# Optimization experiments

Hardware: AMD Instinct MI355X
Metric: run time of the kernel (lower is better)

## Reference

```python
import jax, jax.numpy as jnp
import numpy as np
import math

EMB = 768
B, S = 8, 2048

def setup_inputs() -> dict:
    key = jax.random.key(0)
    ks = jax.random.split(key, 6)
    q = jax.random.normal(ks[0], (B, S, EMB), dtype=jnp.float32)
    k = jax.random.normal(ks[1], (B, S, EMB), dtype=jnp.float32)
    v = jax.random.normal(ks[2], (B, S, EMB), dtype=jnp.float32)
    mask = jax.random.randint(ks[3], (B, S, S), 0, 2, dtype=jnp.int32)
    # nn.Linear(emb, emb): weight [out, in], bias [out]
    bound = 1.0 / math.sqrt(EMB)
    W = jax.random.uniform(ks[4], (EMB, EMB), minval=-bound, maxval=bound, dtype=jnp.float32)
    b = jax.random.uniform(ks[5], (EMB,), minval=-bound, maxval=bound, dtype=jnp.float32)
    return {"q": q, "k": k, "v": v, "mask": mask, "W": W, "b": b}

def reference(q, k, v, mask, W, b):
    # shared linear projection (torch Linear: x @ W^T + b)
    qp = jnp.einsum('bse,oe->bso', q, W) + b
    kp = jnp.einsum('bse,oe->bso', k, W) + b
    vp = jnp.einsum('bse,oe->bso', v, W) + b
    scores = jnp.einsum('bqe,bke->bqk', qp, kp) / math.sqrt(EMB)  # [B,S,S]
    scores = jnp.where(mask == 1, -jnp.inf, scores)
    attn = jax.nn.softmax(scores, axis=-1)
    return jnp.einsum('bqk,bke->bqe', attn, vp)
```

## Files before the change

### kernel.cpp

```cpp
#include <hip/hip_runtime.h>
#include <hip/hip_bf16.h>
#include <stdint.h>

#define B_ 8
#define S_ 2048
#define E_ 768

typedef __attribute__((ext_vector_type(4))) float f32x4;
typedef __attribute__((ext_vector_type(8))) short bf16x8;

#define TILE_USH (256 * 32)

__device__ __forceinline__ unsigned pk2bf(float x, float y) {
  unsigned r;
  asm("v_cvt_pk_bf16_f32 %0, %1, %2" : "=v"(r) : "v"(x), "v"(y));
  return r;
}

__device__ __forceinline__ void gll16(const void* g, void* l) {
  __builtin_amdgcn_global_load_lds((const __attribute__((address_space(1))) void*)g,
                                   (__attribute__((address_space(3))) void*)l, 16, 0, 0);
}

__device__ __forceinline__ void stage_op(const char* Gb, int ld, int kt,
                                         unsigned short* Ls, int tid) {
#pragma unroll
  for (int i = 0; i < 2; ++i) {
    const unsigned lin = (unsigned)i * 8192u + (unsigned)tid * 16u;
    const unsigned row = lin >> 6;
    const unsigned chunk = (lin >> 4) & 3u;
    const unsigned sw = (chunk ^ ((row >> 1) & 3u)) << 4;
    gll16(Gb + (size_t)row * ld + (size_t)kt * 64 + sw, (char*)Ls + lin);
  }
}

__device__ __forceinline__ void ldsA8(const unsigned short* As, int wm, int lane,
                                      bf16x8 (&af)[8]) {
  const unsigned ksw = (unsigned)(lane >> 4);
#pragma unroll
  for (int m = 0; m < 8; ++m) {
    const unsigned row = (unsigned)(wm * 128 + m * 16 + (lane & 15));
    const unsigned off = row * 64 + ((ksw ^ ((row >> 1) & 3u)) << 4);
    af[m] = *reinterpret_cast<const bf16x8*>((const char*)As + off);
  }
}

__device__ __forceinline__ void ldsB2(const unsigned short* Bs, int wn, int n0, int lane,
                                      bf16x8 (&bf)[2]) {
  const unsigned ksw = (unsigned)(lane >> 4);
#pragma unroll
  for (int j = 0; j < 2; ++j) {
    const unsigned row = (unsigned)(wn * 64 + (n0 + j) * 16 + (lane & 15));
    const unsigned off = row * 64 + ((ksw ^ ((row >> 1) & 3u)) << 4);
    bf[j] = *reinterpret_cast<const bf16x8*>((const char*)Bs + off);
  }
}

__device__ __forceinline__ void gemm_pipe32(const char* Ab, const char* Bb, int ldA, int ldB,
                                            int NT, unsigned short* AsAll, unsigned short* BsAll,
                                            int tid, int wm, int wn, int lane,
                                            f32x4 (&acc)[8][4]) {
#pragma unroll
  for (int t = 0; t < 3; ++t) {
    stage_op(Ab, ldA, t, AsAll + t * TILE_USH, tid);
    stage_op(Bb, ldB, t, BsAll + t * TILE_USH, tid);
  }
  asm volatile("s_waitcnt vmcnt(8)" ::: "memory");
  __builtin_amdgcn_s_barrier();
  __builtin_amdgcn_sched_barrier(0);
  for (int kt = 0; kt < NT; ++kt) {
    const int bk = kt & 3;
    const unsigned short* As = AsAll + bk * TILE_USH;
    const unsigned short* Bs = BsAll + bk * TILE_USH;
    const int bs = (kt + 3) & 3;
    bf16x8 af[8], b01[2], b23[2];
    ldsA8(As, wm, lane, af);
    ldsB2(Bs, wn, 0, lane, b01);
    if (kt + 3 < NT) stage_op(Ab, ldA, kt + 3, AsAll + bs * TILE_USH, tid);
    __builtin_amdgcn_s_barrier();
    asm volatile("s_waitcnt lgkmcnt(0)" ::: "memory");
    __builtin_amdgcn_sched_barrier(0);
    __builtin_amdgcn_s_setprio(1);
#pragma unroll
    for (int m = 0; m < 8; ++m) {
      acc[m][0] = __builtin_amdgcn_mfma_f32_16x16x32_bf16(af[m], b01[0], acc[m][0], 0, 0, 0);
      acc[m][1] = __builtin_amdgcn_mfma_f32_16x16x32_bf16(af[m], b01[1], acc[m][1], 0, 0, 0);
    }
    __builtin_amdgcn_s_setprio(0);
    __builtin_amdgcn_s_barrier();
    ldsB2(Bs, wn, 2, lane, b23);
    if (kt + 3 < NT) stage_op(Bb, ldB, kt + 3, BsAll + bs * TILE_USH, tid);
    __builtin_amdgcn_s_barrier();
    asm volatile("s_waitcnt lgkmcnt(0)" ::: "memory");
    __builtin_amdgcn_sched_barrier(0);
    __builtin_amdgcn_s_setprio(1);
#pragma unroll
    for (int m = 0; m < 8; ++m) {
      acc[m][2] = __builtin_amdgcn_mfma_f32_16x16x32_bf16(af[m], b23[0], acc[m][2], 0, 0, 0);
      acc[m][3] = __builtin_amdgcn_mfma_f32_16x16x32_bf16(af[m], b23[1], acc[m][3], 0, 0, 0);
    }
    __builtin_amdgcn_s_setprio(0);
    if (kt + 1 < NT) {
      if (kt + 3 < NT)       asm volatile("s_waitcnt vmcnt(8)" ::: "memory");
      else if (kt + 3 == NT) asm volatile("s_waitcnt vmcnt(4)" ::: "memory");
      else                   asm volatile("s_waitcnt vmcnt(0)" ::: "memory");
      __builtin_amdgcn_s_barrier();
      __builtin_amdgcn_sched_barrier(0);
    }
  }
}

__global__ __launch_bounds__(256) void k_cvt(const float* __restrict__ q,
                                             const float* __restrict__ k,
                                             const float* __restrict__ v,
                                             const float* __restrict__ W,
                                             const int* __restrict__ mask,
                                             unsigned short* __restrict__ qb,
                                             unsigned short* __restrict__ kb,
                                             unsigned short* __restrict__ vb,
                                             unsigned short* __restrict__ Wb,
                                             unsigned long long* __restrict__ mwords) {
  const int y = blockIdx.y;
  if (y == 4) {
    const int nchunks = B_ * S_ * (S_ / 256);
    const int lane = threadIdx.x & 63;
    const int wave = (blockIdx.x * 256 + threadIdx.x) >> 6;
    const int nw = gridDim.x * 4;
    int c = wave;
    for (; c + 3 * nw < nchunks; c += 4 * nw) {
      int4 v0 = *reinterpret_cast<const int4*>(&mask[(size_t)c * 256 + lane * 4]);
      int4 v1 = *reinterpret_cast<const int4*>(&mask[(size_t)(c + nw) * 256 + lane * 4]);
      int4 v2 = *reinterpret_cast<const int4*>(&mask[(size_t)(c + 2 * nw) * 256 + lane * 4]);
      int4 v3 = *reinterpret_cast<const int4*>(&mask[(size_t)(c + 3 * nw) * 256 + lane * 4]);
      unsigned long long a0 = __ballot(v0.x == 1), a1 = __ballot(v0.y == 1);
      unsigned long long a2 = __ballot(v0.z == 1), a3 = __ballot(v0.w == 1);
      unsigned long long b0 = __ballot(v1.x == 1), b1 = __ballot(v1.y == 1);
      unsigned long long b2 = __ballot(v1.z == 1), b3 = __ballot(v1.w == 1);
      unsigned long long c0 = __ballot(v2.x == 1), c1 = __ballot(v2.y == 1);
      unsigned long long c2 = __ballot(v2.z == 1), c3 = __ballot(v2.w == 1);
      unsigned long long d0 = __ballot(v3.x == 1), d1 = __ballot(v3.y == 1);
      unsigned long long d2 = __ballot(v3.z == 1), d3 = __ballot(v3.w == 1);
      if (lane == 0) {
        *reinterpret_cast<ulonglong2*>(&mwords[(size_t)c * 4]) = make_ulonglong2(a0, a1);
        *reinterpret_cast<ulonglong2*>(&mwords[(size_t)c * 4 + 2]) = make_ulonglong2(a2, a3);
        *reinterpret_cast<ulonglong2*>(&mwords[(size_t)(c + nw) * 4]) = make_ulonglong2(b0, b1);
        *reinterpret_cast<ulonglong2*>(&mwords[(size_t)(c + nw) * 4 + 2]) = make_ulonglong2(b2, b3);
        *reinterpret_cast<ulonglong2*>(&mwords[(size_t)(c + 2 * nw) * 4]) = make_ulonglong2(c0, c1);
        *reinterpret_cast<ulonglong2*>(&mwords[(size_t)(c + 2 * nw) * 4 + 2]) = make_ulonglong2(c2, c3);
        *reinterpret_cast<ulonglong2*>(&mwords[(size_t)(c + 3 * nw) * 4]) = make_ulonglong2(d0, d1);
        *reinterpret_cast<ulonglong2*>(&mwords[(size_t)(c + 3 * nw) * 4 + 2]) = make_ulonglong2(d2, d3);
      }
    }
    for (; c < nchunks; c += nw) {
      int4 v0 = *reinterpret_cast<const int4*>(&mask[(size_t)c * 256 + lane * 4]);
      unsigned long long a0 = __ballot(v0.x == 1), a1 = __ballot(v0.y == 1);
      unsigned long long a2 = __ballot(v0.z == 1), a3 = __ballot(v0.w == 1);
      if (lane == 0) {
        *reinterpret_cast<ulonglong2*>(&mwords[(size_t)c * 4]) = make_ulonglong2(a0, a1);
        *reinterpret_cast<ulonglong2*>(&mwords[(size_t)c * 4 + 2]) = make_ulonglong2(a2, a3);
      }
    }
    return;
  }
  const float* src = (y == 0) ? q : (y == 1) ? k : (y == 2) ? v : W;
  unsigned short* dst = (y == 0) ? qb : (y == 1) ? kb : (y == 2) ? vb : Wb;
  const int n4 = (y < 3) ? (B_ * S_ * E_ / 4) : (E_ * E_ / 4);
  const int stride = gridDim.x * 256;
  const float4* s4 = reinterpret_cast<const float4*>(src);
  uint2* d2 = reinterpret_cast<uint2*>(dst);
  int i = blockIdx.x * 256 + threadIdx.x;
  for (; i + 3 * stride < n4; i += 4 * stride) {
    float4 f0 = s4[i];
    float4 f1 = s4[i + stride];
    float4 f2 = s4[i + 2 * stride];
    float4 f3 = s4[i + 3 * stride];
    d2[i]              = make_uint2(pk2bf(f0.x, f0.y), pk2bf(f0.z, f0.w));
    d2[i + stride]     = make_uint2(pk2bf(f1.x, f1.y), pk2bf(f1.z, f1.w));
    d2[i + 2 * stride] = make_uint2(pk2bf(f2.x, f2.y), pk2bf(f2.z, f2.w));
    d2[i + 3 * stride] = make_uint2(pk2bf(f3.x, f3.y), pk2bf(f3.z, f3.w));
  }
  for (; i < n4; i += stride) {
    float4 f0 = s4[i];
    d2[i] = make_uint2(pk2bf(f0.x, f0.y), pk2bf(f0.z, f0.w));
  }
}

__global__ __launch_bounds__(512, 1) void k_projb(const unsigned short* __restrict__ Xb,
                                                  const unsigned short* __restrict__ Wb,
                                                  const float* __restrict__ bias,
                                                  unsigned short* __restrict__ qp,
                                                  unsigned short* __restrict__ kp,
                                                  unsigned short* __restrict__ vp) {
  __shared__ __attribute__((aligned(16))) unsigned short AsAll[4 * TILE_USH];
  __shared__ __attribute__((aligned(16))) unsigned short BsAll[4 * TILE_USH];
  const int tid = threadIdx.x, lane = tid & 63, wid = tid >> 6;
  const int wm = wid >> 2, wn = wid & 3;
  const int c0 = blockIdx.x * 256, r0 = blockIdx.y * 256, z = blockIdx.z;
  const unsigned short* X = Xb + (size_t)z * (B_ * S_ * E_);
  unsigned short* O = (z == 0) ? qp : ((z == 1) ? kp : vp);

  const char* Ab = (const char*)(X + (size_t)r0 * E_);
  const char* Bb = (const char*)(Wb + (size_t)c0 * E_);
  f32x4 acc[8][4] = {};
  gemm_pipe32(Ab, Bb, E_ * 2, E_ * 2, E_ / 32, AsAll, BsAll, tid, wm, wn, lane, acc);

  float bcol[4];
#pragma unroll
  for (int n = 0; n < 4; ++n) bcol[n] = bias[c0 + wn * 64 + n * 16 + (lane & 15)];
#pragma unroll
  for (int m = 0; m < 8; ++m)
#pragma unroll
    for (int r = 0; r < 4; ++r) {
      const int row = r0 + wm * 128 + m * 16 + (lane >> 4) * 4 + r;
#pragma unroll
      for (int n = 0; n < 4; ++n) {
        const int col = c0 + wn * 64 + n * 16 + (lane & 15);
        O[(size_t)row * E_ + col] = (unsigned short)pk2bf(acc[m][n][r] + bcol[n], 0.f);
      }
    }
}

__global__ __launch_bounds__(256) void k_vtrans(const unsigned short* __restrict__ vp,
                                                unsigned short* __restrict__ vpT) {
  __shared__ __attribute__((aligned(16))) unsigned short t[64][72];
  const int tid = threadIdx.x;
  const int st = blockIdx.x;
  const int ot = blockIdx.y;
  const int b = blockIdx.z;
#pragma unroll
  for (int i = 0; i < 2; ++i) {
    int f = i * 256 + tid;
    int s = f >> 3, c8 = f & 7;
    uint4 vv = *reinterpret_cast<const uint4*>(
        &vp[((size_t)b * S_ + st * 64 + s) * E_ + ot * 64 + c8 * 8]);
    *reinterpret_cast<uint4*>(&t[s][c8 * 8]) = vv;
  }
  __syncthreads();
  const int o = tid >> 2;
  const int sb = (tid & 3) * 16;
  unsigned p[8];
#pragma unroll
  for (int j = 0; j < 8; ++j)
    p[j] = (unsigned)t[sb + 2 * j][o] | ((unsigned)t[sb + 2 * j + 1][o] << 16);
  uint4 w0 = make_uint4(p[0], p[1], p[2], p[3]);
  uint4 w1 = make_uint4(p[4], p[5], p[6], p[7]);
  size_t ob = ((size_t)b * E_ + ot * 64 + o) * S_ + st * 64 + sb;
  *reinterpret_cast<uint4*>(&vpT[ob]) = w0;
  *reinterpret_cast<uint4*>(&vpT[ob + 8]) = w1;
}

__global__ __launch_bounds__(512, 1) void k_scores(const unsigned short* __restrict__ qp,
                                                   const unsigned short* __restrict__ kp,
                                                   const unsigned long long* __restrict__ mwords,
                                                   unsigned short* __restrict__ P,
                                                   float* __restrict__ rowsum) {
  __shared__ __attribute__((aligned(16))) unsigned short AsAll[4 * TILE_USH];
  __shared__ __attribute__((aligned(16))) unsigned short BsAll[4 * TILE_USH];
  __shared__ float rlds[256][4];
  const int tid = threadIdx.x, lane = tid & 63, wid = tid >> 6;
  const int wm = wid >> 2, wn = wid & 3;
  const int yt = blockIdx.x, qt = blockIdx.y, b = blockIdx.z;
  const char* Ab = (const char*)(qp + ((size_t)b * S_ + qt * 256) * E_);
  const char* Bb = (const char*)(kp + ((size_t)b * S_ + yt * 256) * E_);
  f32x4 acc[8][4] = {};
  gemm_pipe32(Ab, Bb, E_ * 2, E_ * 2, E_ / 32, AsAll, BsAll, tid, wm, wn, lane, acc);

  const float SC = (float)(1.4426950408889634 / 27.712812921102035);
#pragma unroll
  for (int m = 0; m < 8; ++m)
#pragma unroll
    for (int r = 0; r < 4; ++r) {
      const int rloc = wm * 128 + m * 16 + (lane >> 4) * 4 + r;
      const int grow = qt * 256 + rloc;
      const size_t rowoff = ((size_t)b * S_ + grow) * S_;
      const unsigned long long mw =
          mwords[(((size_t)b * S_ + grow) * 8 + yt) * 4 + (lane & 3)];
      const int shb = wn * 16 + ((lane & 15) >> 2);
      const int cbase = yt * 256 + wn * 64 + (lane & 15);
      float radd = 0.f;
#pragma unroll
      for (int n = 0; n < 4; ++n) {
        float pv = ((mw >> (shb + n * 4)) & 1ull)
                       ? 0.f
                       : __builtin_amdgcn_exp2f(acc[m][n][r] * SC);
        radd += pv;
        P[rowoff + cbase + n * 16] = (unsigned short)pk2bf(pv, 0.f);
      }
      float vsum = radd;
      vsum += __shfl_xor(vsum, 1);
      vsum += __shfl_xor(vsum, 2);
      vsum += __shfl_xor(vsum, 4);
      vsum += __shfl_xor(vsum, 8);
      if ((lane & 15) == 0) rlds[rloc][wn] = vsum;
    }
  __syncthreads();
  if (tid < 256) {
    rowsum[(size_t)yt * (B_ * S_) + (size_t)b * S_ + qt * 256 + tid] =
        (rlds[tid][0] + rlds[tid][1]) + (rlds[tid][2] + rlds[tid][3]);
  }
}

__global__ __launch_bounds__(256) void k_invrs(const float* __restrict__ rowsum,
                                               float* __restrict__ inv_rs) {
  int i = blockIdx.x * 256 + threadIdx.x;
  float t = 0.f;
#pragma unroll
  for (int g = 0; g < 8; ++g) t += rowsum[(size_t)g * (B_ * S_) + i];
  inv_rs[i] = 1.0f / t;
}

__global__ __launch_bounds__(512, 1) void k_pv(const unsigned short* __restrict__ P,
                                               const unsigned short* __restrict__ vpT,
                                               const float* __restrict__ inv_rs,
                                               float* __restrict__ out) {
  __shared__ __attribute__((aligned(16))) unsigned short AsAll[4 * TILE_USH];
  __shared__ __attribute__((aligned(16))) unsigned short BsAll[4 * TILE_USH];
  const int tid = threadIdx.x, lane = tid & 63, wid = tid >> 6;
  const int wm = wid >> 2, wn = wid & 3;
  const int yt = blockIdx.x, mt = blockIdx.y, b = blockIdx.z;
  const char* Ab = (const char*)(P + ((size_t)b * S_ + mt * 256) * S_);
  const char* Bb = (const char*)(vpT + ((size_t)b * E_ + yt * 256) * S_);
  f32x4 acc[8][4] = {};
  gemm_pipe32(Ab, Bb, S_ * 2, S_ * 2, S_ / 32, AsAll, BsAll, tid, wm, wn, lane, acc);

#pragma unroll
  for (int m = 0; m < 8; ++m)
#pragma unroll
    for (int r = 0; r < 4; ++r) {
      const int grow = mt * 256 + wm * 128 + m * 16 + (lane >> 4) * 4 + r;
      const float inv = inv_rs[b * S_ + grow];
#pragma unroll
      for (int n = 0; n < 4; ++n) {
        const int col = yt * 256 + wn * 64 + n * 16 + (lane & 15);
        out[((size_t)b * S_ + grow) * E_ + col] = acc[m][n][r] * inv;
      }
    }
}

extern "C" void kernel_launch(void* const* d_in, const int* in_sizes, int n_in,
                              void* d_out, int out_size, void* d_ws, size_t ws_size,
                              hipStream_t stream) {
  const float* q = (const float*)d_in[0];
  const float* k = (const float*)d_in[1];
  const float* v = (const float*)d_in[2];
  const int* mask = (const int*)d_in[3];
  const float* W = (const float*)d_in[4];
  const float* bias = (const float*)d_in[5];
  float* out = (float*)d_out;
  char* ws = (char*)d_ws;

  unsigned short* qb = (unsigned short*)(ws + 0);
  unsigned short* kb = (unsigned short*)(ws + 25165824);
  unsigned short* vb = (unsigned short*)(ws + 50331648);
  unsigned short* Wb = (unsigned short*)(ws + 75497472);
  unsigned short* qp = (unsigned short*)(ws + 76677120);
  unsigned short* kp = (unsigned short*)(ws + 101842944);
  unsigned short* vpT = (unsigned short*)(ws + 127008768);
  unsigned short* P = (unsigned short*)(ws + 0);
  float* rowsum = (float*)(ws + 75497472);
  float* inv_rs = (float*)(ws + 76546048);
  unsigned short* vp_tmp = (unsigned short*)d_out;
  unsigned long long* mwords =
      (unsigned long long*)((char*)d_out + 25165824);
  (void)in_sizes; (void)n_in; (void)out_size; (void)ws_size;

  dim3 blk(256, 1, 1);
  dim3 blk2(512, 1, 1);
  k_cvt<<<dim3(512, 5, 1), blk, 0, stream>>>(q, k, v, W, mask, qb, kb, vb, Wb, mwords);
  k_projb<<<dim3(3, 64, 3), blk2, 0, stream>>>(qb, Wb, bias, qp, kp, vp_tmp);
  k_vtrans<<<dim3(32, 12, 8), blk, 0, stream>>>(vp_tmp, vpT);
  k_scores<<<dim3(8, 8, 8), blk2, 0, stream>>>(qp, kp, mwords, P, rowsum);
  k_invrs<<<dim3(64, 1, 1), blk, 0, stream>>>(rowsum, inv_rs);
  k_pv<<<dim3(3, 8, 8), blk2, 0, stream>>>(P, vpT, inv_rs, out);
}
```

Before: 327.0 us.

## Switch GEMMs to 128x128 tiles with double buffering and 3 blocks per CU

Replaces the 256x256-tile, 512-thread, 4-stage GEMM pipeline with a 128x128 tile, 256-thread, 2-stage double-buffered loop used by the projection, scores and PV kernels. Grids grow fourfold and launch bounds allow 3 blocks per CU, aiming for more occupancy and better wave balance across CUs. Mask word indexing and the rowsum partial count (8 to 16) are adjusted to the new tile width. The trade is lower arithmetic intensity per tile, more global/L2 traffic, and a shallower prefetch that fully drains vmcnt each iteration.

```diff
diff --git a/kernel.cpp b/kernel.cpp
--- a/kernel.cpp
+++ b/kernel.cpp
@@ -9,7 +9,6 @@
 typedef __attribute__((ext_vector_type(4))) float f32x4;
 typedef __attribute__((ext_vector_type(8))) short bf16x8;
 
-#define TILE_USH (256 * 32)
 
 __device__ __forceinline__ unsigned pk2bf(float x, float y) {
   unsigned r;
@@ -22,88 +21,67 @@
                                    (__attribute__((address_space(3))) void*)l, 16, 0, 0);
 }
 
-__device__ __forceinline__ void stage_op(const char* Gb, int ld, int kt,
-                                         unsigned short* Ls, int tid) {
+__device__ __forceinline__ void gemm128(const char* __restrict__ Ab,
+                                        const char* __restrict__ Bb,
+                                        int ldA, int ldB, int NT,
+                                        unsigned short* As, unsigned short* Bs,
+                                        int tid, int wm, int wn, int lane,
+                                        f32x4 (&acc)[4][4]) {
+  unsigned sA[2], sB[2], lin2[2];
 #pragma unroll
   for (int i = 0; i < 2; ++i) {
-    const unsigned lin = (unsigned)i * 8192u + (unsigned)tid * 16u;
-    const unsigned row = lin >> 6;
-    const unsigned chunk = (lin >> 4) & 3u;
-    const unsigned sw = (chunk ^ ((row >> 1) & 3u)) << 4;
-    gll16(Gb + (size_t)row * ld + (size_t)kt * 64 + sw, (char*)Ls + lin);
-  }
-}
-
-__device__ __forceinline__ void ldsA8(const unsigned short* As, int wm, int lane,
-                                      bf16x8 (&af)[8]) {
-  const unsigned ksw = (unsigned)(lane >> 4);
-#pragma unroll
-  for (int m = 0; m < 8; ++m) {
-    const unsigned row = (unsigned)(wm * 128 + m * 16 + (lane & 15));
-    const unsigned off = row * 64 + ((ksw ^ ((row >> 1) & 3u)) << 4);
-    af[m] = *reinterpret_cast<const bf16x8*>((const char*)As + off);
-  }
-}
-
-__device__ __forceinline__ void ldsB2(const unsigned short* Bs, int wn, int n0, int lane,
-                                      bf16x8 (&bf)[2]) {
-  const unsigned ksw = (unsigned)(lane >> 4);
-#pragma unroll
-  for (int j = 0; j < 2; ++j) {
-    const unsigned row = (unsigned)(wn * 64 + (n0 + j) * 16 + (lane & 15));
-    const unsigned off = row * 64 + ((ksw ^ ((row >> 1) & 3u)) << 4);
-    bf[j] = *reinterpret_cast<const bf16x8*>((const char*)Bs + off);
-  }
-}
-
-__device__ __forceinline__ void gemm_pipe32(const char* Ab, const char* Bb, int ldA, int ldB,
-                                            int NT, unsigned short* AsAll, unsigned short* BsAll,
-                                            int tid, int wm, int wn, int lane,
-                                            f32x4 (&acc)[8][4]) {
-#pragma unroll
-  for (int t = 0; t < 3; ++t) {
-    stage_op(Ab, ldA, t, AsAll + t * TILE_USH, tid);
-    stage_op(Bb, ldB, t, BsAll + t * TILE_USH, tid);
-  }
-  asm volatile("s_waitcnt vmcnt(8)" ::: "memory");
+    const unsigned lin = (unsigned)i * 4096u + (unsigned)tid * 16u;
+    const unsigned row = lin >> 6, ch = (lin >> 4) & 3u;
+    const unsigned sw = (ch ^ ((row >> 1) & 3u)) << 4;
+    sA[i] = row * (unsigned)ldA + sw;
+    sB[i] = row * (unsigned)ldB + sw;
+    lin2[i] = lin;
+  }
+  unsigned aoff[4], boff[4];
+#pragma unroll
+  for (int m = 0; m < 4; ++m) {
+    unsigned row = (unsigned)(wm * 64 + m * 16 + (lane & 15));
+    aoff[m] = row * 64 + ((((unsigned)lane >> 4) ^ ((row >> 1) & 3u)) << 4);
+    row = (unsigned)(wn * 64 + m * 16 + (lane & 15));
+    boff[m] = row * 64 + ((((unsigned)lane >> 4) ^ ((row >> 1) & 3u)) << 4);
+  }
+#pragma unroll
+  for (int i = 0; i < 2; ++i) {
+    gll16(Ab + sA[i], (char*)As + lin2[i]);
+    gll16(Bb + sB[i], (char*)Bs + lin2[i]);
+  }
+  asm volatile("s_waitcnt vmcnt(0)" ::: "memory");
   __builtin_amdgcn_s_barrier();
   __builtin_amdgcn_sched_barrier(0);
   for (int kt = 0; kt < NT; ++kt) {
-    const int bk = kt & 3;
-    const unsigned short* As = AsAll + bk * TILE_USH;
-    const unsigned short* Bs = BsAll + bk * TILE_USH;
-    const int bs = (kt + 3) & 3;
-    bf16x8 af[8], b01[2], b23[2];
-    ldsA8(As, wm, lane, af);
-    ldsB2(Bs, wn, 0, lane, b01);
-    if (kt + 3 < NT) stage_op(Ab, ldA, kt + 3, AsAll + bs * TILE_USH, tid);
-    __builtin_amdgcn_s_barrier();
+    const char* Ac = (const char*)As + (kt & 1) * 8192;
+    const char* Bc = (const char*)Bs + (kt & 1) * 8192;
+    char* An = (char*)As + ((kt + 1) & 1) * 8192;
+    char* Bn = (char*)Bs + ((kt + 1) & 1) * 8192;
+    if (kt + 1 < NT) {
+      const size_t ko = (size_t)(kt + 1) * 64;
+#pragma unroll
+      for (int i = 0; i < 2; ++i) {
+        gll16(Ab + sA[i] + ko, An + lin2[i]);
+        gll16(Bb + sB[i] + ko, Bn + lin2[i]);
+      }
+    }
+    bf16x8 af[4], bf[4];
+#pragma unroll
+    for (int m = 0; m < 4; ++m) af[m] = *reinterpret_cast<const bf16x8*>(Ac + aoff[m]);
+#pragma unroll
+    for (int n = 0; n < 4; ++n) bf[n] = *reinterpret_cast<const bf16x8*>(Bc + boff[n]);
     asm volatile("s_waitcnt lgkmcnt(0)" ::: "memory");
     __builtin_amdgcn_sched_barrier(0);
     __builtin_amdgcn_s_setprio(1);
 #pragma unroll
-    for (int m = 0; m < 8; ++m) {
-      acc[m][0] = __builtin_amdgcn_mfma_f32_16x16x32_bf16(af[m], b01[0], acc[m][0], 0, 0, 0);
-      acc[m][1] = __builtin_amdgcn_mfma_f32_16x16x32_bf16(af[m], b01[1], acc[m][1], 0, 0, 0);
-    }
-    __builtin_amdgcn_s_setprio(0);
-    __builtin_amdgcn_s_barrier();
-    ldsB2(Bs, wn, 2, lane, b23);
-    if (kt + 3 < NT) stage_op(Bb, ldB, kt + 3, BsAll + bs * TILE_USH, tid);
-    __builtin_amdgcn_s_barrier();
-    asm volatile("s_waitcnt lgkmcnt(0)" ::: "memory");
-    __builtin_amdgcn_sched_barrier(0);
-    __builtin_amdgcn_s_setprio(1);
-#pragma unroll
-    for (int m = 0; m < 8; ++m) {
-      acc[m][2] = __builtin_amdgcn_mfma_f32_16x16x32_bf16(af[m], b23[0], acc[m][2], 0, 0, 0);
-      acc[m][3] = __builtin_amdgcn_mfma_f32_16x16x32_bf16(af[m], b23[1], acc[m][3], 0, 0, 0);
-    }
+    for (int m = 0; m < 4; ++m)
+#pragma unroll
+      for (int n = 0; n < 4; ++n)
+        acc[m][n] = __builtin_amdgcn_mfma_f32_16x16x32_bf16(af[m], bf[n], acc[m][n], 0, 0, 0);
     __builtin_amdgcn_s_setprio(0);
     if (kt + 1 < NT) {
-      if (kt + 3 < NT)       asm volatile("s_waitcnt vmcnt(8)" ::: "memory");
-      else if (kt + 3 == NT) asm volatile("s_waitcnt vmcnt(4)" ::: "memory");
-      else                   asm volatile("s_waitcnt vmcnt(0)" ::: "memory");
+      asm volatile("s_waitcnt vmcnt(0)" ::: "memory");
       __builtin_amdgcn_s_barrier();
       __builtin_amdgcn_sched_barrier(0);
     }
@@ -185,33 +163,32 @@
   }
 }
 
-__global__ __launch_bounds__(512, 1) void k_projb(const unsigned short* __restrict__ Xb,
+__global__ __launch_bounds__(256, 3) void k_projb(const unsigned short* __restrict__ Xb,
                                                   const unsigned short* __restrict__ Wb,
                                                   const float* __restrict__ bias,
                                                   unsigned short* __restrict__ qp,
                                                   unsigned short* __restrict__ kp,
                                                   unsigned short* __restrict__ vp) {
-  __shared__ __attribute__((aligned(16))) unsigned short AsAll[4 * TILE_USH];
-  __shared__ __attribute__((aligned(16))) unsigned short BsAll[4 * TILE_USH];
+  __shared__ __attribute__((aligned(16))) unsigned short As[2 * 4096];
+  __shared__ __attribute__((aligned(16))) unsigned short Bs[2 * 4096];
   const int tid = threadIdx.x, lane = tid & 63, wid = tid >> 6;
-  const int wm = wid >> 2, wn = wid & 3;
-  const int c0 = blockIdx.x * 256, r0 = blockIdx.y * 256, z = blockIdx.z;
+  const int wm = wid >> 1, wn = wid & 1;
+  const int c0 = blockIdx.x * 128, r0 = blockIdx.y * 128, z = blockIdx.z;
   const unsigned short* X = Xb + (size_t)z * (B_ * S_ * E_);
   unsigned short* O = (z == 0) ? qp : ((z == 1) ? kp : vp);
 
-  const char* Ab = (const char*)(X + (size_t)r0 * E_);
-  const char* Bb = (const char*)(Wb + (size_t)c0 * E_);
-  f32x4 acc[8][4] = {};
-  gemm_pipe32(Ab, Bb, E_ * 2, E_ * 2, E_ / 32, AsAll, BsAll, tid, wm, wn, lane, acc);
+  f32x4 acc[4][4] = {};
+  gemm128((const char*)(X + (size_t)r0 * E_), (const char*)(Wb + (size_t)c0 * E_),
+          E_ * 2, E_ * 2, E_ / 32, As, Bs, tid, wm, wn, lane, acc);
 
   float bcol[4];
 #pragma unroll
   for (int n = 0; n < 4; ++n) bcol[n] = bias[c0 + wn * 64 + n * 16 + (lane & 15)];
 #pragma unroll
-  for (int m = 0; m < 8; ++m)
+  for (int m = 0; m < 4; ++m)
 #pragma unroll
     for (int r = 0; r < 4; ++r) {
-      const int row = r0 + wm * 128 + m * 16 + (lane >> 4) * 4 + r;
+      const int row = r0 + wm * 64 + m * 16 + (lane >> 4) * 4 + r;
 #pragma unroll
       for (int n = 0; n < 4; ++n) {
         const int col = c0 + wn * 64 + n * 16 + (lane & 15);
@@ -249,34 +226,34 @@
   *reinterpret_cast<uint4*>(&vpT[ob + 8]) = w1;
 }
 
-__global__ __launch_bounds__(512, 1) void k_scores(const unsigned short* __restrict__ qp,
+__global__ __launch_bounds__(256, 3) void k_scores(const unsigned short* __restrict__ qp,
                                                    const unsigned short* __restrict__ kp,
                                                    const unsigned long long* __restrict__ mwords,
                                                    unsigned short* __restrict__ P,
                                                    float* __restrict__ rowsum) {
-  __shared__ __attribute__((aligned(16))) unsigned short AsAll[4 * TILE_USH];
-  __shared__ __attribute__((aligned(16))) unsigned short BsAll[4 * TILE_USH];
-  __shared__ float rlds[256][4];
+  __shared__ __attribute__((aligned(16))) unsigned short As[2 * 4096];
+  __shared__ __attribute__((aligned(16))) unsigned short Bs[2 * 4096];
+  __shared__ float rlds[128][2];
   const int tid = threadIdx.x, lane = tid & 63, wid = tid >> 6;
-  const int wm = wid >> 2, wn = wid & 3;
+  const int wm = wid >> 1, wn = wid & 1;
   const int yt = blockIdx.x, qt = blockIdx.y, b = blockIdx.z;
-  const char* Ab = (const char*)(qp + ((size_t)b * S_ + qt * 256) * E_);
-  const char* Bb = (const char*)(kp + ((size_t)b * S_ + yt * 256) * E_);
-  f32x4 acc[8][4] = {};
-  gemm_pipe32(Ab, Bb, E_ * 2, E_ * 2, E_ / 32, AsAll, BsAll, tid, wm, wn, lane, acc);
+  f32x4 acc[4][4] = {};
+  gemm128((const char*)(qp + ((size_t)b * S_ + qt * 128) * E_),
+          (const char*)(kp + ((size_t)b * S_ + yt * 128) * E_),
+          E_ * 2, E_ * 2, E_ / 32, As, Bs, tid, wm, wn, lane, acc);
 
   const float SC = (float)(1.4426950408889634 / 27.712812921102035);
 #pragma unroll
-  for (int m = 0; m < 8; ++m)
+  for (int m = 0; m < 4; ++m)
 #pragma unroll
     for (int r = 0; r < 4; ++r) {
-      const int rloc = wm * 128 + m * 16 + (lane >> 4) * 4 + r;
-      const int grow = qt * 256 + rloc;
+      const int rloc = wm * 64 + m * 16 + (lane >> 4) * 4 + r;
+      const int grow = qt * 128 + rloc;
       const size_t rowoff = ((size_t)b * S_ + grow) * S_;
       const unsigned long long mw =
-          mwords[(((size_t)b * S_ + grow) * 8 + yt) * 4 + (lane & 3)];
-      const int shb = wn * 16 + ((lane & 15) >> 2);
-      const int cbase = yt * 256 + wn * 64 + (lane & 15);
+          mwords[(((size_t)b * S_ + grow) * 8 + (yt >> 1)) * 4 + (lane & 3)];
+      const int shb = (yt & 1) * 32 + wn * 16 + ((lane & 15) >> 2);
+      const int cbase = yt * 128 + wn * 64 + (lane & 15);
       float radd = 0.f;
 #pragma unroll
       for (int n = 0; n < 4; ++n) {
@@ -294,9 +271,9 @@
       if ((lane & 15) == 0) rlds[rloc][wn] = vsum;
     }
   __syncthreads();
-  if (tid < 256) {
-    rowsum[(size_t)yt * (B_ * S_) + (size_t)b * S_ + qt * 256 + tid] =
-        (rlds[tid][0] + rlds[tid][1]) + (rlds[tid][2] + rlds[tid][3]);
+  if (tid < 128) {
+    rowsum[(size_t)yt * (B_ * S_) + (size_t)b * S_ + qt * 128 + tid] =
+        rlds[tid][0] + rlds[tid][1];
   }
 }
 
@@ -305,33 +282,33 @@
   int i = blockIdx.x * 256 + threadIdx.x;
   float t = 0.f;
 #pragma unroll
-  for (int g = 0; g < 8; ++g) t += rowsum[(size_t)g * (B_ * S_) + i];
+  for (int g = 0; g < 16; ++g) t += rowsum[(size_t)g * (B_ * S_) + i];
   inv_rs[i] = 1.0f / t;
 }
 
-__global__ __launch_bounds__(512, 1) void k_pv(const unsigned short* __restrict__ P,
+__global__ __launch_bounds__(256, 3) void k_pv(const unsigned short* __restrict__ P,
                                                const unsigned short* __restrict__ vpT,
                                                const float* __restrict__ inv_rs,
                                                float* __restrict__ out) {
-  __shared__ __attribute__((aligned(16))) unsigned short AsAll[4 * TILE_USH];
-  __shared__ __attribute__((aligned(16))) unsigned short BsAll[4 * TILE_USH];
+  __shared__ __attribute__((aligned(16))) unsigned short As[2 * 4096];
+  __shared__ __attribute__((aligned(16))) unsigned short Bs[2 * 4096];
   const int tid = threadIdx.x, lane = tid & 63, wid = tid >> 6;
-  const int wm = wid >> 2, wn = wid & 3;
-  const int yt = blockIdx.x, mt = blockIdx.y, b = blockIdx.z;
-  const char* Ab = (const char*)(P + ((size_t)b * S_ + mt * 256) * S_);
-  const char* Bb = (const char*)(vpT + ((size_t)b * E_ + yt * 256) * S_);
-  f32x4 acc[8][4] = {};
-  gemm_pipe32(Ab, Bb, S_ * 2, S_ * 2, S_ / 32, AsAll, BsAll, tid, wm, wn, lane, acc);
-
-#pragma unroll
-  for (int m = 0; m < 8; ++m)
+  const int wm = wid >> 1, wn = wid & 1;
+  const int et = blockIdx.x, mt = blockIdx.y, b = blockIdx.z;
+  f32x4 acc[4][4] = {};
+  gemm128((const char*)(P + ((size_t)b * S_ + mt * 128) * S_),
+          (const char*)(vpT + ((size_t)b * E_ + et * 128) * S_),
+          S_ * 2, S_ * 2, S_ / 32, As, Bs, tid, wm, wn, lane, acc);
+
+#pragma unroll
+  for (int m = 0; m < 4; ++m)
 #pragma unroll
     for (int r = 0; r < 4; ++r) {
-      const int grow = mt * 256 + wm * 128 + m * 16 + (lane >> 4) * 4 + r;
+      const int grow = mt * 128 + wm * 64 + m * 16 + (lane >> 4) * 4 + r;
       const float inv = inv_rs[b * S_ + grow];
 #pragma unroll
       for (int n = 0; n < 4; ++n) {
-        const int col = yt * 256 + wn * 64 + n * 16 + (lane & 15);
+        const int col = et * 128 + wn * 64 + n * 16 + (lane & 15);
         out[((size_t)b * S_ + grow) * E_ + col] = acc[m][n][r] * inv;
       }
     }
@@ -365,11 +342,10 @@
   (void)in_sizes; (void)n_in; (void)out_size; (void)ws_size;
 
   dim3 blk(256, 1, 1);
-  dim3 blk2(512, 1, 1);
   k_cvt<<<dim3(512, 5, 1), blk, 0, stream>>>(q, k, v, W, mask, qb, kb, vb, Wb, mwords);
-  k_projb<<<dim3(3, 64, 3), blk2, 0, stream>>>(qb, Wb, bias, qp, kp, vp_tmp);
+  k_projb<<<dim3(6, 128, 3), blk, 0, stream>>>(qb, Wb, bias, qp, kp, vp_tmp);
   k_vtrans<<<dim3(32, 12, 8), blk, 0, stream>>>(vp_tmp, vpT);
-  k_scores<<<dim3(8, 8, 8), blk2, 0, stream>>>(qp, kp, mwords, P, rowsum);
+  k_scores<<<dim3(16, 16, 8), blk, 0, stream>>>(qp, kp, mwords, P, rowsum);
   k_invrs<<<dim3(64, 1, 1), blk, 0, stream>>>(rowsum, inv_rs);
-  k_pv<<<dim3(3, 8, 8), blk2, 0, stream>>>(P, vpT, inv_rs, out);
-}
+  k_pv<<<dim3(6, 16, 8), blk, 0, stream>>>(P, vpT, inv_rs, out);
+}
```

New measurement: 351.9 us. 7.6% more time.
